# Kernel tuning notes

Hardware: AMD Instinct MI355X
Metric: run time of the kernel (lower is better)

Reference implementation:

```python
import jax, jax.numpy as jnp
import numpy as np

N, D, H, Z = 131072, 224, 400, 4
TOPK = 20


def _init_linear(key, fan_in, fan_out):
    kw, kb = jax.random.split(key)
    bound = 1.0 / np.sqrt(fan_in)
    W = jax.random.uniform(kw, (fan_in, fan_out), jnp.float32, -bound, bound)
    b = jax.random.uniform(kb, (fan_out,), jnp.float32, -bound, bound)
    return W, b


def setup_inputs() -> dict:
    key = jax.random.key(0)
    ks = jax.random.split(key, 8)
    We1, be1 = _init_linear(ks[0], D, H)
    We2, be2 = _init_linear(ks[1], H, H)
    We3, be3 = _init_linear(ks[2], H, Z)
    Wd1, bd1 = _init_linear(ks[3], Z, H)
    Wd2, bd2 = _init_linear(ks[4], H, H)
    Wd3, bd3 = _init_linear(ks[5], H, D)
    x = jax.random.normal(ks[6], (N, D), dtype=jnp.float32)
    data_input = jax.random.normal(ks[7], (D, 1), dtype=jnp.float32)
    return {
        "x": x, "data_input": data_input,
        "We1": We1, "be1": be1, "We2": We2, "be2": be2, "We3": We3, "be3": be3,
        "Wd1": Wd1, "bd1": bd1, "Wd2": Wd2, "bd2": bd2, "Wd3": Wd3, "bd3": bd3,
    }


def _lrelu(v):
    return jnp.where(v > 0, v, 0.1 * v)  # leaky_relu slope 0.1


def reference(x, data_input, We1, be1, We2, be2, We3, be3, Wd1, bd1, Wd2, bd2, Wd3, bd3):
    # encoder
    h = _lrelu(x @ We1 + be1)
    h = _lrelu(h @ We2 + be2)
    z = h @ We3 + be3                       # [N, Z]
    # decoder
    g = _lrelu(z @ Wd1 + bd1)
    g = _lrelu(g @ Wd2 + bd2)
    y = jnp.tanh(g @ Wd3 + bd3)             # [N, D]
    # my_loss, vectorized: per-sample cosine similarity of y[i] with the
    # reference spectrum data_input, then topk(k=20) over the batch.
    d = data_input[:, 0]                     # [D]
    A = y @ d                                # [N]  (sum(y[i]*d))
    B = jnp.linalg.norm(y, axis=1)           # [N]
    C = jnp.linalg.norm(d)
    defen = A / (B * C + 1e-5)               # [N]
    s, _ = jax.lax.top_k(defen, TOPK)
    sam_loss = jnp.sum(s)
    mse_loss = jnp.mean((y - x) ** 2)        # F.mse_loss default mean reduction
    R_loss = mse_loss + 0.1 * sam_loss       # sum/mean of a scalar is a no-op
    return y, z, R_loss
```

## Files before the change

### kernel.cpp

```cpp
#include <hip/hip_runtime.h>
#include <hip/hip_bf16.h>
#include <math.h>

typedef _Float16 f16x8 __attribute__((ext_vector_type(8)));
typedef float f32x4 __attribute__((ext_vector_type(4)));
typedef unsigned int u32;
typedef unsigned short u16;

#define NROWS 131072
#define DDIM 224
#define HREAL 400
#define HP 416
#define ROWS 32
#define PROW 832
#define PLANE 26624
#define LDS_TOTAL 53248

#define OFF_W1    0
#define OFF_W2    186368
#define OFF_W5    532480
#define OFF_W6    878592
#define OFF_W3    1064960
#define OFF_W4    1078272
#define OFF_C     1104896
#define OFF_MSEP  1104912
#define OFF_DEFEN 1121296
#define OFF_CAND  1645584

__device__ __forceinline__ u16 f2h(float v) {
  union { _Float16 h; u16 u; } c;
  c.h = (_Float16)v;
  return c.u;
}

__device__ __forceinline__ void pack8(int i, int NKS, int KREAL, int NREAL, int NLD,
                                      const float* __restrict__ W,
                                      u16* __restrict__ Wo) {
  const int e = i & 7, l15 = (i >> 3) & 15, g = (i >> 7) & 3;
  const int rest = i >> 9;
  const int ks = rest % NKS, nb = rest / NKS;
  const int n = nb * 16 + l15, k = ks * 32 + g * 8 + e;
  const float w = (n < NREAL && k < KREAL) ? W[k * NLD + n] : 0.f;
  Wo[i] = f2h(w);
}

__global__ void k_prep(const float* __restrict__ We1, const float* __restrict__ We2,
                       const float* __restrict__ Wd2, const float* __restrict__ Wd3,
                       const float* __restrict__ We3, const float* __restrict__ Wd1,
                       const float* __restrict__ dvec,
                       u16* __restrict__ W1, u16* __restrict__ W2,
                       u16* __restrict__ W5, u16* __restrict__ W6,
                       u16* __restrict__ W3, u16* __restrict__ W4,
                       float* __restrict__ Cout) {
  const int t = blockIdx.x * 256 + threadIdx.x;
  const int NT = gridDim.x * 256;
  for (int i = t; i < 26 * 7 * 512;  i += NT) pack8(i, 7,  DDIM,  HREAL, HREAL, We1, W1);
  for (int i = t; i < 26 * 13 * 512; i += NT) pack8(i, 13, HREAL, HREAL, HREAL, We2, W2);
  for (int i = t; i < 26 * 13 * 512; i += NT) pack8(i, 13, HREAL, HREAL, HREAL, Wd2, W5);
  for (int i = t; i < 14 * 13 * 512; i += NT) pack8(i, 13, HREAL, DDIM,  DDIM,  Wd3, W6);
  for (int i = t; i < 1 * 13 * 512;  i += NT) pack8(i, 13, HREAL, 4,     4,     We3, W3);
  for (int i = t; i < 26 * 1 * 512;  i += NT) pack8(i, 1,  4,     HREAL, HREAL, Wd1, W4);
  if (blockIdx.x == 0) {
    float s = 0.f;
    for (int i = threadIdx.x; i < DDIM; i += 256) { float v = dvec[i]; s += v * v; }
#pragma unroll
    for (int off = 1; off < 64; off <<= 1) s += __shfl_xor(s, off);
    __shared__ float cs[4];
    if ((threadIdx.x & 63) == 0) cs[threadIdx.x >> 6] = s;
    __syncthreads();
    if (threadIdx.x == 0) Cout[0] = sqrtf(cs[0] + cs[1] + cs[2] + cs[3]);
  }
}

template <int NKS, int NFW>
__device__ __forceinline__ void gemmN(const char* ip, const u16* __restrict__ W,
                                      int nb0, int l15, int g, f32x4 (&acc)[2][NFW]) {
  const int lof = (g << 7) + (l15 << 3);
  const int gs = g ^ (l15 & 3);
  const char* a0b = ip + l15 * PROW + gs * 16;
  const char* a1b = a0b + 16 * PROW;
  const u16* wp[NFW];
#pragma unroll
  for (int nf = 0; nf < NFW; ++nf)
    wp[nf] = W + ((((size_t)(nb0 + nf) * NKS) << 9) + lof);
  f16x8 b[NFW][3];
#pragma unroll
  for (int nf = 0; nf < NFW; ++nf) b[nf][0] = *(const f16x8*)wp[nf];
  if (NKS > 1) {
#pragma unroll
    for (int nf = 0; nf < NFW; ++nf) b[nf][1] = *(const f16x8*)(wp[nf] + 512);
  }
#pragma unroll
  for (int ks = 0; ks < NKS; ++ks) {
    const int cur = ks % 3;
    if (ks + 2 < NKS) {
      const int nxt = (ks + 2) % 3;
#pragma unroll
      for (int nf = 0; nf < NFW; ++nf)
        b[nf][nxt] = *(const f16x8*)(wp[nf] + (size_t)(ks + 2) * 512);
    }
    const f16x8 a0 = *(const f16x8*)(a0b + ks * 64);
    const f16x8 a1 = *(const f16x8*)(a1b + ks * 64);
    __builtin_amdgcn_s_setprio(1);
#pragma unroll
    for (int nf = 0; nf < NFW; ++nf) {
      acc[0][nf] = __builtin_amdgcn_mfma_f32_16x16x32_f16(a0, b[nf][cur], acc[0][nf], 0, 0, 0);
      acc[1][nf] = __builtin_amdgcn_mfma_f32_16x16x32_f16(a1, b[nf][cur], acc[1][nf], 0, 0, 0);
    }
    __builtin_amdgcn_s_setprio(0);
  }
}

__device__ __forceinline__ void epi2(f32x4 (&acc)[2][2], const float* __restrict__ bias,
                                     int nb0, char* op, int l15, int g) {
#pragma unroll
  for (int nf = 0; nf < 2; ++nf) {
    const int col = (nb0 + nf) * 16 + l15;
    const float bv = (col < HREAL) ? bias[col] : 0.f;
    const int cu = col >> 3;
    const int crem = (col & 7) * 2;
#pragma unroll
    for (int mf = 0; mf < 2; ++mf) {
#pragma unroll
      for (int j = 0; j < 4; ++j) {
        const int row = mf * 16 + g * 4 + j;
        float v = acc[mf][nf][j] + bv;
        v = fmaxf(v, 0.1f * v);
        *(u16*)(op + row * PROW + ((cu ^ (row & 3)) << 4) + crem) = f2h(v);
      }
    }
  }
}

__global__ __launch_bounds__(256, 3) void k_main(
    const float* __restrict__ xin, const float* __restrict__ dvec,
    const float* __restrict__ be1, const float* __restrict__ be2, const float* __restrict__ be3,
    const float* __restrict__ bd1, const float* __restrict__ bd2, const float* __restrict__ bd3,
    const u16* __restrict__ W1, const u16* __restrict__ W2,
    const u16* __restrict__ W5, const u16* __restrict__ W6,
    const u16* __restrict__ W3, const u16* __restrict__ W4,
    const float* __restrict__ Cptr,
    float* __restrict__ y_out, float* __restrict__ z_out,
    float* __restrict__ defen, float* __restrict__ msep) {
  extern __shared__ __align__(16) char lds[];
  char* pa = lds;
  char* pb = lds + PLANE;

  const int tid = threadIdx.x;
  const int lane = tid & 63;
  const int wid = tid >> 6;
  const int l15 = lane & 15;
  const int g = lane >> 4;
  const size_t row0 = (size_t)blockIdx.x * ROWS;

#pragma unroll
  for (int i = 0; i < 7; ++i) {
    const int f = i * 256 + tid;
    const int r = f / 56, c4 = f - r * 56;
    const float4 v = *(const float4*)(xin + (row0 + r) * DDIM + c4 * 4);
    const float vv[4] = {v.x, v.y, v.z, v.w};
    ushort4 hh;
    u16* hw = (u16*)&hh;
#pragma unroll
    for (int w = 0; w < 4; ++w) hw[w] = f2h(vv[w]);
    *(ushort4*)(pa + r * PROW + (((c4 >> 1) ^ (r & 3)) << 4) + (c4 & 1) * 8) = hh;
  }
  __syncthreads();

  for (int c = wid; c < 13; c += 4) {
    f32x4 acc[2][2] = {};
    gemmN<7, 2>(pa, W1, 2 * c, l15, g, acc);
    epi2(acc, be1, 2 * c, pb, l15, g);
  }
  __syncthreads();

  for (int c = wid; c < 13; c += 4) {
    f32x4 acc[2][2] = {};
    gemmN<13, 2>(pb, W2, 2 * c, l15, g, acc);
    epi2(acc, be2, 2 * c, pa, l15, g);
  }
  __syncthreads();

  if (wid == 0) {
    f32x4 acc3[2][1] = {};
    gemmN<13, 1>(pa, W3, 0, l15, g, acc3);
    float zv[2][4];
#pragma unroll
    for (int mf = 0; mf < 2; ++mf) {
#pragma unroll
      for (int j = 0; j < 4; ++j) {
        const float s = acc3[mf][0][j] + ((l15 < 4) ? be3[l15] : 0.f);
        zv[mf][j] = s;
        if (l15 < 4) z_out[(row0 + mf * 16 + g * 4 + j) * 4 + l15] = s;
      }
    }
#pragma unroll
    for (int mf = 0; mf < 2; ++mf) {
#pragma unroll
      for (int j = 0; j < 4; ++j) {
        const float z0 = __shfl(zv[mf][j], (lane & ~15) + 0);
        const float z1 = __shfl(zv[mf][j], (lane & ~15) + 1);
        const float z2 = __shfl(zv[mf][j], (lane & ~15) + 2);
        const float z3 = __shfl(zv[mf][j], (lane & ~15) + 3);
        if (l15 < 4) {
          const int r = mf * 16 + g * 4 + j;
          uint4 zq = {0u, 0u, 0u, 0u};
          if (l15 == 0) {
            zq.x = (u32)f2h(z0) | ((u32)f2h(z1) << 16);
            zq.y = (u32)f2h(z2) | ((u32)f2h(z3) << 16);
          }
          *(uint4*)(pb + r * PROW + ((l15 ^ (r & 3)) << 4)) = zq;
        }
      }
    }
  }
  __syncthreads();

  for (int c = wid; c < 13; c += 4) {
    f32x4 acc[2][2] = {};
    gemmN<1, 2>(pb, W4, 2 * c, l15, g, acc);
    epi2(acc, bd1, 2 * c, pa, l15, g);
  }
  __syncthreads();

  for (int c = wid; c < 13; c += 4) {
    f32x4 acc[2][2] = {};
    gemmN<13, 2>(pa, W5, 2 * c, l15, g, acc);
    epi2(acc, bd2, 2 * c, pb, l15, g);
  }
  __syncthreads();

  {
    float pA[2][4] = {}, pB[2][4] = {}, pM[2][4] = {};
    for (int c = wid; c < 7; c += 4) {
      const int nb0 = 2 * c;
      f32x4 acc[2][2] = {};
      gemmN<13, 2>(pb, W6, nb0, l15, g, acc);
#pragma unroll
      for (int mf = 0; mf < 2; ++mf) {
#pragma unroll
        for (int j = 0; j < 4; ++j) {
          const size_t grow = row0 + mf * 16 + g * 4 + j;
#pragma unroll
          for (int nf = 0; nf < 2; ++nf) {
            const int col = (nb0 + nf) * 16 + l15;
            const float v = acc[mf][nf][j] + bd3[col];
            const float e = __expf(2.f * v);
            const float y = 1.f - 2.f * __builtin_amdgcn_rcpf(e + 1.f);
            y_out[grow * DDIM + col] = y;
            pA[mf][j] = fmaf(y, dvec[col], pA[mf][j]);
            pB[mf][j] = fmaf(y, y, pB[mf][j]);
            const float df = y - xin[grow * DDIM + col];
            pM[mf][j] = fmaf(df, df, pM[mf][j]);
          }
        }
      }
    }
    float* red = (float*)pa;
#pragma unroll
    for (int mf = 0; mf < 2; ++mf) {
#pragma unroll
      for (int j = 0; j < 4; ++j) {
        float a = pA[mf][j], b = pB[mf][j], m = pM[mf][j];
#pragma unroll
        for (int off = 1; off < 16; off <<= 1) {
          a += __shfl_xor(a, off);
          b += __shfl_xor(b, off);
          m += __shfl_xor(m, off);
        }
        if (l15 == 0) {
          const int lrow = mf * 16 + g * 4 + j;
          red[(lrow * 4 + wid) * 4 + 0] = a;
          red[(lrow * 4 + wid) * 4 + 1] = b;
          red[(lrow * 4 + wid) * 4 + 2] = m;
        }
      }
    }
  }
  __syncthreads();

  if (tid < 32) {
    const float Cn = Cptr[0];
    const float* red = (const float*)pa;
    float A = 0.f, B2 = 0.f, M = 0.f;
#pragma unroll
    for (int w = 0; w < 4; ++w) {
      A  += red[(tid * 4 + w) * 4 + 0];
      B2 += red[(tid * 4 + w) * 4 + 1];
      M  += red[(tid * 4 + w) * 4 + 2];
    }
    defen[row0 + tid] = A / (sqrtf(B2) * Cn + 1e-5f);
#pragma unroll
    for (int off = 1; off < 32; off <<= 1) M += __shfl_xor(M, off);
    if (tid == 0) msep[blockIdx.x] = M;
  }
}

__global__ void k_topk_a(const float* __restrict__ defen, float* __restrict__ cand) {
  __shared__ float vals[2048];
  __shared__ float wv[4];
  __shared__ int wi[4];
  const int tid = threadIdx.x;
  const int base = blockIdx.x * 2048;
  for (int i = tid; i < 2048; i += 256) vals[i] = defen[base + i];
  __syncthreads();
  for (int it = 0; it < 20; ++it) {
    float mv = -1e30f; int mi = 1 << 30;
    for (int i = tid; i < 2048; i += 256) {
      float v = vals[i];
      if (v > mv) { mv = v; mi = i; }
    }
#pragma unroll
    for (int off = 1; off < 64; off <<= 1) {
      float ov = __shfl_xor(mv, off); int oi = __shfl_xor(mi, off);
      if (ov > mv || (ov == mv && oi < mi)) { mv = ov; mi = oi; }
    }
    if ((tid & 63) == 0) { wv[tid >> 6] = mv; wi[tid >> 6] = mi; }
    __syncthreads();
    if (tid == 0) {
      float bv = wv[0]; int bi = wi[0];
      for (int q = 1; q < 4; ++q)
        if (wv[q] > bv || (wv[q] == bv && wi[q] < bi)) { bv = wv[q]; bi = wi[q]; }
      cand[blockIdx.x * 20 + it] = bv;
      vals[bi] = -1e30f;
    }
    __syncthreads();
  }
}

__global__ void k_topk_b(const float* __restrict__ cand, const float* __restrict__ msep,
                         float* __restrict__ rloss) {
  __shared__ float vals[1280];
  __shared__ float wv[4];
  __shared__ int wi[4];
  __shared__ float msum[4];
  const int tid = threadIdx.x;
  for (int i = tid; i < 1280; i += 256) vals[i] = cand[i];
  float ms = 0.f;
  for (int i = tid; i < 4096; i += 256) ms += msep[i];
#pragma unroll
  for (int off = 1; off < 64; off <<= 1) ms += __shfl_xor(ms, off);
  if ((tid & 63) == 0) msum[tid >> 6] = ms;
  __syncthreads();
  float sam = 0.f;
  for (int it = 0; it < 20; ++it) {
    float mv = -1e30f; int mi = 1 << 30;
    for (int i = tid; i < 1280; i += 256) {
      float v = vals[i];
      if (v > mv) { mv = v; mi = i; }
    }
#pragma unroll
    for (int off = 1; off < 64; off <<= 1) {
      float ov = __shfl_xor(mv, off); int oi = __shfl_xor(mi, off);
      if (ov > mv || (ov == mv && oi < mi)) { mv = ov; mi = oi; }
    }
    if ((tid & 63) == 0) { wv[tid >> 6] = mv; wi[tid >> 6] = mi; }
    __syncthreads();
    if (tid == 0) {
      float bv = wv[0]; int bi = wi[0];
      for (int q = 1; q < 4; ++q)
        if (wv[q] > bv || (wv[q] == bv && wi[q] < bi)) { bv = wv[q]; bi = wi[q]; }
      sam += bv;
      vals[bi] = -1e30f;
    }
    __syncthreads();
  }
  if (tid == 0) {
    float mse = (msum[0] + msum[1] + msum[2] + msum[3]) / 29360128.f;
    rloss[0] = mse + 0.1f * sam;
  }
}

extern "C" void kernel_launch(void* const* d_in, const int* in_sizes, int n_in,
                              void* d_out, int out_size, void* d_ws, size_t ws_size,
                              hipStream_t stream) {
  const float* x    = (const float*)d_in[0];
  const float* dinp = (const float*)d_in[1];
  const float* We1  = (const float*)d_in[2];
  const float* be1  = (const float*)d_in[3];
  const float* We2  = (const float*)d_in[4];
  const float* be2  = (const float*)d_in[5];
  const float* We3  = (const float*)d_in[6];
  const float* be3  = (const float*)d_in[7];
  const float* Wd1  = (const float*)d_in[8];
  const float* bd1  = (const float*)d_in[9];
  const float* Wd2  = (const float*)d_in[10];
  const float* bd2  = (const float*)d_in[11];
  const float* Wd3  = (const float*)d_in[12];
  const float* bd3  = (const float*)d_in[13];

  float* y_out = (float*)d_out;
  float* z_out = y_out + (size_t)NROWS * DDIM;
  float* r_out = z_out + (size_t)NROWS * 4;

  char* ws = (char*)d_ws;
  u16* W1 = (u16*)(ws + OFF_W1);
  u16* W2 = (u16*)(ws + OFF_W2);
  u16* W5 = (u16*)(ws + OFF_W5);
  u16* W6 = (u16*)(ws + OFF_W6);
  u16* W3 = (u16*)(ws + OFF_W3);
  u16* W4 = (u16*)(ws + OFF_W4);
  float* Cf    = (float*)(ws + OFF_C);
  float* msep  = (float*)(ws + OFF_MSEP);
  float* defen = (float*)(ws + OFF_DEFEN);
  float* cand  = (float*)(ws + OFF_CAND);

  (void)hipFuncSetAttribute((const void*)k_main, hipFuncAttributeMaxDynamicSharedMemorySize, LDS_TOTAL);

  k_prep<<<dim3(256), dim3(256), 0, stream>>>(We1, We2, Wd2, Wd3, We3, Wd1, dinp,
                                              W1, W2, W5, W6, W3, W4, Cf);
  k_main<<<dim3(4096), dim3(256), LDS_TOTAL, stream>>>(x, dinp, be1, be2, be3, bd1, bd2, bd3,
                                                       W1, W2, W5, W6, W3, W4,
                                                       Cf, y_out, z_out, defen, msep);
  k_topk_a<<<dim3(64), dim3(256), 0, stream>>>(defen, cand);
  k_topk_b<<<dim3(1), dim3(256), 0, stream>>>(cand, msep, r_out);
}
```

Baseline: 306.2 us.

## Widen per-wave GEMM column tiles from 2 to 4 fragments

Each wave now computes four 16-column fragments per pass instead of two, so every A-fragment LDS load is reused across more MFMAs and there are fewer loop passes per layer. The last layer is split so waves 0-2 take four fragments and wave 3 takes two. The cost is more accumulator and B-buffer registers, which may pressure the 3-blocks-per-CU occupancy target. Load balance also shifts: in 7-chunk layers, waves 0-2 do two chunks while wave 3 does one.

```diff
diff --git a/kernel.cpp b/kernel.cpp
--- a/kernel.cpp
+++ b/kernel.cpp
@@ -111,10 +111,11 @@
   }
 }
 
-__device__ __forceinline__ void epi2(f32x4 (&acc)[2][2], const float* __restrict__ bias,
+template <int NFW>
+__device__ __forceinline__ void epiN(f32x4 (&acc)[2][NFW], const float* __restrict__ bias,
                                      int nb0, char* op, int l15, int g) {
 #pragma unroll
-  for (int nf = 0; nf < 2; ++nf) {
+  for (int nf = 0; nf < NFW; ++nf) {
     const int col = (nb0 + nf) * 16 + l15;
     const float bv = (col < HREAL) ? bias[col] : 0.f;
     const int cu = col >> 3;
@@ -127,6 +128,56 @@
         float v = acc[mf][nf][j] + bv;
         v = fmaxf(v, 0.1f * v);
         *(u16*)(op + row * PROW + ((cu ^ (row & 3)) << 4) + crem) = f2h(v);
+      }
+    }
+  }
+}
+
+template <int NKS>
+__device__ __forceinline__ void layerN(const char* ip, char* op,
+                                       const u16* __restrict__ W,
+                                       const float* __restrict__ bias,
+                                       int wid, int l15, int g) {
+  for (int ci = wid; ci < 7; ci += 4) {
+    const int nb0 = 4 * ci;
+    if (ci == 6) {
+      f32x4 acc[2][2] = {};
+      gemmN<NKS, 2>(ip, W, nb0, l15, g, acc);
+      epiN<2>(acc, bias, nb0, op, l15, g);
+    } else {
+      f32x4 acc[2][4] = {};
+      gemmN<NKS, 4>(ip, W, nb0, l15, g, acc);
+      epiN<4>(acc, bias, nb0, op, l15, g);
+    }
+  }
+}
+
+template <int NFW>
+__device__ __forceinline__ void l6N(const char* ip, const u16* __restrict__ W6,
+                                    const float* __restrict__ bd3,
+                                    const float* __restrict__ dvec,
+                                    const float* __restrict__ xin,
+                                    float* __restrict__ y_out,
+                                    size_t row0, int nb0, int l15, int g,
+                                    float (&pA)[2][4], float (&pB)[2][4], float (&pM)[2][4]) {
+  f32x4 acc[2][NFW] = {};
+  gemmN<13, NFW>(ip, W6, nb0, l15, g, acc);
+#pragma unroll
+  for (int mf = 0; mf < 2; ++mf) {
+#pragma unroll
+    for (int j = 0; j < 4; ++j) {
+      const size_t grow = row0 + mf * 16 + g * 4 + j;
+#pragma unroll
+      for (int nf = 0; nf < NFW; ++nf) {
+        const int col = (nb0 + nf) * 16 + l15;
+        const float v = acc[mf][nf][j] + bd3[col];
+        const float e = __expf(2.f * v);
+        const float y = 1.f - 2.f * __builtin_amdgcn_rcpf(e + 1.f);
+        y_out[grow * DDIM + col] = y;
+        pA[mf][j] = fmaf(y, dvec[col], pA[mf][j]);
+        pB[mf][j] = fmaf(y, y, pB[mf][j]);
+        const float df = y - xin[grow * DDIM + col];
+        pM[mf][j] = fmaf(df, df, pM[mf][j]);
       }
     }
   }
@@ -167,18 +218,10 @@
   }
   __syncthreads();
 
-  for (int c = wid; c < 13; c += 4) {
-    f32x4 acc[2][2] = {};
-    gemmN<7, 2>(pa, W1, 2 * c, l15, g, acc);
-    epi2(acc, be1, 2 * c, pb, l15, g);
-  }
-  __syncthreads();
-
-  for (int c = wid; c < 13; c += 4) {
-    f32x4 acc[2][2] = {};
-    gemmN<13, 2>(pb, W2, 2 * c, l15, g, acc);
-    epi2(acc, be2, 2 * c, pa, l15, g);
-  }
+  layerN<7>(pa, pb, W1, be1, wid, l15, g);
+  __syncthreads();
+
+  layerN<13>(pb, pa, W2, be2, wid, l15, g);
   __syncthreads();
 
   if (wid == 0) {
@@ -216,46 +259,16 @@
   }
   __syncthreads();
 
-  for (int c = wid; c < 13; c += 4) {
-    f32x4 acc[2][2] = {};
-    gemmN<1, 2>(pb, W4, 2 * c, l15, g, acc);
-    epi2(acc, bd1, 2 * c, pa, l15, g);
-  }
-  __syncthreads();
-
-  for (int c = wid; c < 13; c += 4) {
-    f32x4 acc[2][2] = {};
-    gemmN<13, 2>(pa, W5, 2 * c, l15, g, acc);
-    epi2(acc, bd2, 2 * c, pb, l15, g);
-  }
+  layerN<1>(pb, pa, W4, bd1, wid, l15, g);
+  __syncthreads();
+
+  layerN<13>(pa, pb, W5, bd2, wid, l15, g);
   __syncthreads();
 
   {
     float pA[2][4] = {}, pB[2][4] = {}, pM[2][4] = {};
-    for (int c = wid; c < 7; c += 4) {
-      const int nb0 = 2 * c;
-      f32x4 acc[2][2] = {};
-      gemmN<13, 2>(pb, W6, nb0, l15, g, acc);
-#pragma unroll
-      for (int mf = 0; mf < 2; ++mf) {
-#pragma unroll
-        for (int j = 0; j < 4; ++j) {
-          const size_t grow = row0 + mf * 16 + g * 4 + j;
-#pragma unroll
-          for (int nf = 0; nf < 2; ++nf) {
-            const int col = (nb0 + nf) * 16 + l15;
-            const float v = acc[mf][nf][j] + bd3[col];
-            const float e = __expf(2.f * v);
-            const float y = 1.f - 2.f * __builtin_amdgcn_rcpf(e + 1.f);
-            y_out[grow * DDIM + col] = y;
-            pA[mf][j] = fmaf(y, dvec[col], pA[mf][j]);
-            pB[mf][j] = fmaf(y, y, pB[mf][j]);
-            const float df = y - xin[grow * DDIM + col];
-            pM[mf][j] = fmaf(df, df, pM[mf][j]);
-          }
-        }
-      }
-    }
+    if (wid < 3) l6N<4>(pb, W6, bd3, dvec, xin, y_out, row0, 4 * wid, l15, g, pA, pB, pM);
+    else         l6N<2>(pb, W6, bd3, dvec, xin, y_out, row0, 12,      l15, g, pA, pB, pM);
     float* red = (float*)pa;
 #pragma unroll
     for (int mf = 0; mf < 2; ++mf) {
```

Measured after the change: 332.1 us (median of 2 runs). 8.5% more time.
